# Optimization experiments

Hardware: AMD Instinct MI355X
Metric: run time of the kernel (lower is better)

The kernel has to match this reference:

```python
import jax, jax.numpy as jnp
import numpy as np

NEG_INF = -1000000.0  # matches the original's -1e6 masking constant


def setup_inputs() -> dict:
    key = jax.random.key(0)
    ks = jax.random.split(key, 7)
    B, S, A, Q, D = 32, 2048, 1024, 1024, 1024  # batch, src len, attend_dim, query_dim, att_dim
    return {
        "input": jax.random.normal(ks[0], (B, 1, Q), dtype=jnp.float32),
        "context": jax.random.normal(ks[1], (B, S, A), dtype=jnp.float32),
        "W_pre": jax.random.normal(ks[2], (D, A), dtype=jnp.float32) * 0.02,
        "b_pre": jax.random.normal(ks[3], (D,), dtype=jnp.float32) * 0.02,
        "W_q": jax.random.normal(ks[4], (D, Q), dtype=jnp.float32) * 0.02,
        "v": jax.random.normal(ks[5], (D,), dtype=jnp.float32) * 0.02,
        "mask": jax.random.randint(ks[6], (B, 1, S), 0, 2, dtype=jnp.int32),
    }


def reference(input, context, W_pre, b_pre, W_q, v, mask):
    # precompute = linear_pre(context): [B, S, D]
    precompute = jnp.einsum("bsa,da->bsd", context, W_pre) + b_pre
    # targetT = linear_q(input): [B, 1, D]; repeat over S via broadcast
    targetT = jnp.einsum("bqc,dc->bqd", input, W_q)
    tmp = jnp.tanh(precompute + targetT)                 # [B, S, D]
    energy = jnp.einsum("bsd,d->bs", tmp, v)             # linear_v -> [B, S]
    # mask: positions where mask == 0 get -1e6 (energy*(1-m) + m*(-1e6), m = (mask==0))
    masked_out = (mask[:, 0, :] == 0)
    energy = jnp.where(masked_out, NEG_INF, energy)
    score = jax.nn.softmax(energy, axis=1)               # softmax over S
    score_m = score[:, None, :]                          # [B, 1, S]
    weightedContext = jnp.einsum("bqs,bsa->bqa", score_m, context)  # [B, 1, A]
    return weightedContext, score_m, precompute
```

## Files before the change

### kernel.cpp

```cpp
#include <hip/hip_runtime.h>

#define NEG_INF_VAL -1000000.0f

typedef short s16x8 __attribute__((ext_vector_type(8)));
typedef float f32x4 __attribute__((ext_vector_type(4)));

__device__ __forceinline__ unsigned int bf16_rne(float f) {
  unsigned int u = __float_as_uint(f);
  return (u + 0x7fffu + ((u >> 16) & 1u)) >> 16;
}
__device__ __forceinline__ unsigned int pack_bf2(float a, float b) {
  return bf16_rne(a) | (bf16_rne(b) << 16);
}

__device__ __forceinline__ float fast_tanh(float x) {
  float xc = fminf(fmaxf(x, -15.f), 15.f);
  float t = __expf(2.f * xc);
  return __fdividef(t - 1.f, t + 1.f);
}

__global__ __launch_bounds__(256) void convert_bf16_kernel(
    const float* __restrict__ src, unsigned short* __restrict__ dst, long n) {
  long i = ((long)blockIdx.x * blockDim.x + threadIdx.x) * 8;
  long stride = (long)gridDim.x * blockDim.x * 8;
  for (; i < n; i += stride) {
    float4 f0 = *(const float4*)(src + i);
    float4 f1 = *(const float4*)(src + i + 4);
    uint4 o;
    o.x = pack_bf2(f0.x, f0.y);
    o.y = pack_bf2(f0.z, f0.w);
    o.z = pack_bf2(f1.x, f1.y);
    o.w = pack_bf2(f1.z, f1.w);
    *(uint4*)(dst + i) = o;
  }
}

__global__ __launch_bounds__(256) void targetT_kernel(
    const float* __restrict__ input, const float* __restrict__ Wq,
    float* __restrict__ tT) {
  int d0 = blockIdx.x * 8;
  int t = threadIdx.x;
  int b = t >> 3, dl = t & 7;
  __shared__ float in_s[32][32];
  __shared__ float wq_s[8][32];
  float acc = 0.f;
  for (int q0 = 0; q0 < 1024; q0 += 32) {
    int r = t >> 3, c = (t & 7) * 4;
    *(float4*)&in_s[r][c] = *(const float4*)&input[r * 1024 + q0 + c];
    wq_s[t >> 5][t & 31] = Wq[(long)(d0 + (t >> 5)) * 1024 + q0 + (t & 31)];
    __syncthreads();
#pragma unroll
    for (int qq = 0; qq < 32; ++qq)
      acc += in_s[b][qq] * wq_s[dl][qq];
    __syncthreads();
  }
  tT[b * 1024 + d0 + dl] = acc;
}

__device__ __forceinline__ void load_lds16(const void* g, void* l) {
  __builtin_amdgcn_global_load_lds(
      (const __attribute__((address_space(1))) void*)g,
      (__attribute__((address_space(3))) void*)l, 16, 0, 0);
}

#define MFMA_ROW(QI, I, AF)                                                          \
  acc[(QI)*4+(I)][0] = __builtin_amdgcn_mfma_f32_16x16x32_bf16(AF, bf0, acc[(QI)*4+(I)][0], 0, 0, 0); \
  acc[(QI)*4+(I)][1] = __builtin_amdgcn_mfma_f32_16x16x32_bf16(AF, bf1, acc[(QI)*4+(I)][1], 0, 0, 0); \
  acc[(QI)*4+(I)][2] = __builtin_amdgcn_mfma_f32_16x16x32_bf16(AF, bf2, acc[(QI)*4+(I)][2], 0, 0, 0); \
  acc[(QI)*4+(I)][3] = __builtin_amdgcn_mfma_f32_16x16x32_bf16(AF, bf3, acc[(QI)*4+(I)][3], 0, 0, 0);

#define STAGE(SB, SM, SK, SKTREL)                                                    \
  {                                                                                  \
    const unsigned short* gp = ((SM) ? Bg : Ag) + (SKTREL) * 64 + (SK) * 32;         \
    char* lp = dstB + (SB) * 65536 + (SM) * 32768 + (SK) * 16384;                    \
    load_lds16(gp, lp);                                                              \
    load_lds16(gp + 128L * 1024, lp + 8192);                                         \
  }

#define PHASE(BUF, QI, KK, LOADB, SB, SM, SK, SKTREL, VM)                            \
  {                                                                                  \
    const unsigned short* pA = (BUF) ? pA1 : pA0;                                    \
    const unsigned short* pB = (BUF) ? pB1 : pB0;                                    \
    s16x8 af0 = *(const s16x8*)(pA + (KK)*8192 + ((QI)*64 +  0)*32);                 \
    s16x8 af1 = *(const s16x8*)(pA + (KK)*8192 + ((QI)*64 + 16)*32);                 \
    s16x8 af2 = *(const s16x8*)(pA + (KK)*8192 + ((QI)*64 + 32)*32);                 \
    s16x8 af3 = *(const s16x8*)(pA + (KK)*8192 + ((QI)*64 + 48)*32);                 \
    if (LOADB) {                                                                     \
      bf0 = *(const s16x8*)(pB + (KK)*8192 +  0*32);                                 \
      bf1 = *(const s16x8*)(pB + (KK)*8192 + 16*32);                                 \
      bf2 = *(const s16x8*)(pB + (KK)*8192 + 32*32);                                 \
      bf3 = *(const s16x8*)(pB + (KK)*8192 + 48*32);                                 \
    }                                                                                \
    STAGE(SB, SM, SK, SKTREL)                                                        \
    asm volatile("s_waitcnt lgkmcnt(0)" ::: "memory");                               \
    __builtin_amdgcn_sched_barrier(0);                                               \
    __builtin_amdgcn_s_setprio(1);                                                   \
    MFMA_ROW(QI, 0, af0)                                                             \
    MFMA_ROW(QI, 1, af1)                                                             \
    MFMA_ROW(QI, 2, af2)                                                             \
    MFMA_ROW(QI, 3, af3)                                                             \
    __builtin_amdgcn_s_setprio(0);                                                   \
    if (VM) asm volatile("s_waitcnt vmcnt(8)" ::: "memory");                         \
    __builtin_amdgcn_s_barrier();                                                    \
  }

__global__ __launch_bounds__(512, 2) void gemm_energy_kernel(
    const unsigned short* __restrict__ A,
    const unsigned short* __restrict__ Bm,
    const float* __restrict__ b_pre,
    const float* __restrict__ tT,
    const float* __restrict__ vvec,
    float* __restrict__ Cout,
    float* __restrict__ epart) {
  int lin = blockIdx.x;
  int w = (lin & 7) * 128 + (lin >> 3);
  int nt = w & 3;
  int mt = w >> 2;
  int m0 = mt * 256, n0 = nt * 256;
  int tid = threadIdx.x;
  int lane = tid & 63, wid = tid >> 6;
  int wr = wid >> 2, wc = wid & 3;
  int r = lane & 15, g = lane >> 4;

  __shared__ unsigned short sMem[2 * 2 * 2 * 256 * 32];

  f32x4 acc[8][4] = {};
  s16x8 bf0, bf1, bf2, bf3;

  int physoff = (g ^ ((r >> 1) & 3)) * 8;

  int aoffe = (wr * 128 + r) * 32 + physoff;
  int boffe = (wc * 64 + r) * 32 + physoff;
  const unsigned short* pA0 = sMem + aoffe;
  const unsigned short* pA1 = sMem + 32768 + aoffe;
  const unsigned short* pB0 = sMem + 16384 + boffe;
  const unsigned short* pB1 = sMem + 49152 + boffe;
  char* dstB = (char*)sMem + wid * 1024;

  int srow = tid >> 2;
  int slog8 = ((tid & 3) ^ ((tid >> 3) & 3)) * 8;
  const unsigned short* Abase = A + (long)(m0 + srow) * 1024 + slog8;
  const unsigned short* Bbase = Bm + (long)(n0 + srow) * 1024 + slog8;
  const unsigned short* Ag = Abase;
  const unsigned short* Bg = Bbase;

  STAGE(0, 0, 0, 0) STAGE(0, 1, 0, 0)
  STAGE(0, 0, 1, 0) STAGE(0, 1, 1, 0)
  STAGE(1, 0, 0, 1) STAGE(1, 1, 0, 1)
  asm volatile("s_waitcnt vmcnt(8)" ::: "memory");
  __builtin_amdgcn_s_barrier();

#pragma unroll 1
  for (int t0 = 0; t0 < 16; t0 += 2) {
    Ag = Abase + t0 * 64;
    Bg = Bbase + t0 * 64;
    PHASE(0, 0, 0, 1, 1, 0, 1, 1, 0)
    PHASE(0, 1, 0, 0, 1, 1, 1, 1, 1)
    PHASE(0, 0, 1, 1, 0, 0, 0, 2, 0)
    PHASE(0, 1, 1, 0, 0, 1, 0, 2, 1)
    PHASE(1, 0, 0, 1, 0, 0, 1, 2, 0)
    PHASE(1, 1, 0, 0, 0, 1, 1, 2, 1)
    PHASE(1, 0, 1, 1, 1, 0, 0, 3, 0)
    PHASE(1, 1, 1, 0, 1, 1, 0, 3, 1)
  }

  int b = m0 >> 11;
  float bias[4], tv[4], vv[4];
#pragma unroll
  for (int j = 0; j < 4; ++j) {
    int d = n0 + wc * 64 + j * 16 + r;
    bias[j] = b_pre[d];
    tv[j] = tT[b * 1024 + d];
    vv[j] = vvec[d];
  }
#pragma unroll
  for (int i = 0; i < 8; ++i) {
#pragma unroll
    for (int q = 0; q < 4; ++q) {
      int m = m0 + wr * 128 + i * 16 + g * 4 + q;
      float e = 0.f;
#pragma unroll
      for (int j = 0; j < 4; ++j) {
        float val = acc[i][j][q] + bias[j];
        Cout[(long)m * 1024 + n0 + wc * 64 + j * 16 + r] = val;
        e += fast_tanh(val + tv[j]) * vv[j];
      }
      e += __shfl_xor(e, 1);
      e += __shfl_xor(e, 2);
      e += __shfl_xor(e, 4);
      e += __shfl_xor(e, 8);
      if (r == 0) epart[(long)m * 16 + nt * 4 + wc] = e;
    }
  }
}

__global__ __launch_bounds__(256) void softmax_kernel(
    const float* __restrict__ epart, const int* __restrict__ mask,
    float* __restrict__ score) {
  int b = blockIdx.x;
  int t = threadIdx.x;
  __shared__ float red[256];
  float ev[8];
  float mx = -3.4e38f;
#pragma unroll
  for (int ii = 0; ii < 8; ++ii) {
    int s = ii * 256 + t;
    long m = (long)b * 2048 + s;
    const float4* p = (const float4*)(epart + m * 16);
    float4 p0 = p[0], p1 = p[1], p2 = p[2], p3 = p[3];
    float e = p0.x + p0.y + p0.z + p0.w + p1.x + p1.y + p1.z + p1.w
            + p2.x + p2.y + p2.z + p2.w + p3.x + p3.y + p3.z + p3.w;
    if (mask[b * 2048 + s] == 0) e = NEG_INF_VAL;
    ev[ii] = e;
    mx = fmaxf(mx, e);
  }
  red[t] = mx; __syncthreads();
  for (int off = 128; off > 0; off >>= 1) {
    if (t < off) red[t] = fmaxf(red[t], red[t + off]);
    __syncthreads();
  }
  mx = red[0];
  __syncthreads();
  float sum = 0.f;
#pragma unroll
  for (int ii = 0; ii < 8; ++ii) { ev[ii] = __expf(ev[ii] - mx); sum += ev[ii]; }
  red[t] = sum; __syncthreads();
  for (int off = 128; off > 0; off >>= 1) {
    if (t < off) red[t] += red[t + off];
    __syncthreads();
  }
  float inv = 1.f / red[0];
#pragma unroll
  for (int ii = 0; ii < 8; ++ii)
    score[b * 2048 + ii * 256 + t] = ev[ii] * inv;
}

__global__ __launch_bounds__(256) void wc_partial_kernel(
    const unsigned short* __restrict__ ctx, const float* __restrict__ score,
    float* __restrict__ part) {
  int b = blockIdx.x, sc = blockIdx.y;
  int t = threadIdx.x;
  __shared__ float ssc[64];
  if (t < 64) ssc[t] = score[b * 2048 + sc * 64 + t];
  __syncthreads();
  float acc0 = 0.f, acc1 = 0.f, acc2 = 0.f, acc3 = 0.f;
  const unsigned short* cp = ctx + ((long)b * 2048 + sc * 64) * 1024 + t * 4;
  for (int s = 0; s < 64; ++s) {
    uint2 pk = *(const uint2*)cp;
    cp += 1024;
    float wgt = ssc[s];
    acc0 += wgt * __uint_as_float(pk.x << 16);
    acc1 += wgt * __uint_as_float(pk.x & 0xffff0000u);
    acc2 += wgt * __uint_as_float(pk.y << 16);
    acc3 += wgt * __uint_as_float(pk.y & 0xffff0000u);
  }
  float* pp = part + ((long)(b * 32 + sc)) * 1024 + t * 4;
  pp[0] = acc0; pp[1] = acc1; pp[2] = acc2; pp[3] = acc3;
}

__global__ __launch_bounds__(256) void wc_reduce_kernel(
    const float* __restrict__ part, float* __restrict__ wc) {
  int id = blockIdx.x * 256 + threadIdx.x;
  int b = id >> 10, a = id & 1023;
  float s = 0.f;
#pragma unroll
  for (int scn = 0; scn < 32; ++scn)
    s += part[((long)(b * 32 + scn)) * 1024 + a];
  wc[id] = s;
}

extern "C" void kernel_launch(void* const* d_in, const int* in_sizes, int n_in,
                              void* d_out, int out_size, void* d_ws, size_t ws_size,
                              hipStream_t stream) {
  const float* input   = (const float*)d_in[0];
  const float* context = (const float*)d_in[1];
  const float* W_pre   = (const float*)d_in[2];
  const float* b_pre   = (const float*)d_in[3];
  const float* W_q     = (const float*)d_in[4];
  const float* v       = (const float*)d_in[5];
  const int*   mask    = (const int*)d_in[6];

  float* out       = (float*)d_out;
  float* out_wc    = out;
  float* out_score = out + 32768;
  float* out_pre   = out + 98304;

  const size_t OFF_CTX   = 0;
  const size_t OFF_WPRE  = 134217728;
  const size_t OFF_TT    = 136314880;
  const size_t OFF_EPART = 136445952;
  const size_t OFF_WCP   = 140640256;
  const size_t WS_NEED   = 144834560;
  if (ws_size < WS_NEED) return;

  char* ws = (char*)d_ws;
  unsigned short* ctx_bf  = (unsigned short*)(ws + OFF_CTX);
  unsigned short* wpre_bf = (unsigned short*)(ws + OFF_WPRE);
  float* tT     = (float*)(ws + OFF_TT);
  float* epart  = (float*)(ws + OFF_EPART);
  float* wcpart = (float*)(ws + OFF_WCP);

  convert_bf16_kernel<<<2048, 256, 0, stream>>>(context, ctx_bf, 64LL * 1024 * 1024);
  convert_bf16_kernel<<<256, 256, 0, stream>>>(W_pre, wpre_bf, 1024LL * 1024);
  targetT_kernel<<<128, 256, 0, stream>>>(input, W_q, tT);
  gemm_energy_kernel<<<1024, 512, 0, stream>>>(ctx_bf, wpre_bf, b_pre, tT, v,
                                               out_pre, epart);
  softmax_kernel<<<32, 256, 0, stream>>>(epart, mask, out_score);
  dim3 g5(32, 32);
  wc_partial_kernel<<<g5, 256, 0, stream>>>(ctx_bf, out_score, wcpart);
  wc_reduce_kernel<<<128, 256, 0, stream>>>(wcpart, out_wc);
}
```

Before: 339.8 us.

## Software-pipeline LDS fragment reads one phase ahead of MFMAs in GEMM

Restructures the GEMM main loop so that A/B fragments for the next phase are read from LDS into a second register set while the MFMAs of the current phase run. This removes the explicit lgkmcnt(0) wait and sched_barrier before each MFMA block, hiding LDS latency behind compute. The global-to-LDS prefetch wait is also loosened from vmcnt(8) to vmcnt(4), and a final vmcnt(0) is added after the loop. The cost is more VGPRs for the double fragment sets, which risks spills or reduced occupancy under the 512x2 launch bounds, and correctness depends on the barrier ordering now that reads run one phase ahead.

```diff
diff --git a/kernel.cpp b/kernel.cpp
--- a/kernel.cpp
+++ b/kernel.cpp
@@ -63,44 +63,44 @@
       (__attribute__((address_space(3))) void*)l, 16, 0, 0);
 }
 
-#define MFMA_ROW(QI, I, AF)                                                          \
-  acc[(QI)*4+(I)][0] = __builtin_amdgcn_mfma_f32_16x16x32_bf16(AF, bf0, acc[(QI)*4+(I)][0], 0, 0, 0); \
-  acc[(QI)*4+(I)][1] = __builtin_amdgcn_mfma_f32_16x16x32_bf16(AF, bf1, acc[(QI)*4+(I)][1], 0, 0, 0); \
-  acc[(QI)*4+(I)][2] = __builtin_amdgcn_mfma_f32_16x16x32_bf16(AF, bf2, acc[(QI)*4+(I)][2], 0, 0, 0); \
-  acc[(QI)*4+(I)][3] = __builtin_amdgcn_mfma_f32_16x16x32_bf16(AF, bf3, acc[(QI)*4+(I)][3], 0, 0, 0);
-
-#define STAGE(SB, SM, SK, SKTREL)                                                    \
+#define RD_A(SET, BUF, KK, QI)                                                       \
+  SET##_0 = *(const s16x8*)(((BUF) ? pA1 : pA0) + (KK)*8192 + ((QI)*64 +  0)*32);    \
+  SET##_1 = *(const s16x8*)(((BUF) ? pA1 : pA0) + (KK)*8192 + ((QI)*64 + 16)*32);    \
+  SET##_2 = *(const s16x8*)(((BUF) ? pA1 : pA0) + (KK)*8192 + ((QI)*64 + 32)*32);    \
+  SET##_3 = *(const s16x8*)(((BUF) ? pA1 : pA0) + (KK)*8192 + ((QI)*64 + 48)*32);
+
+#define RD_B(SET, BUF, KK)                                                           \
+  SET##_0 = *(const s16x8*)(((BUF) ? pB1 : pB0) + (KK)*8192 +  0*32);                \
+  SET##_1 = *(const s16x8*)(((BUF) ? pB1 : pB0) + (KK)*8192 + 16*32);                \
+  SET##_2 = *(const s16x8*)(((BUF) ? pB1 : pB0) + (KK)*8192 + 32*32);                \
+  SET##_3 = *(const s16x8*)(((BUF) ? pB1 : pB0) + (KK)*8192 + 48*32);
+
+#define MFMA_ROW(QI, I, AF, BS)                                                      \
+  acc[(QI)*4+(I)][0] = __builtin_amdgcn_mfma_f32_16x16x32_bf16(AF, BS##_0, acc[(QI)*4+(I)][0], 0, 0, 0); \
+  acc[(QI)*4+(I)][1] = __builtin_amdgcn_mfma_f32_16x16x32_bf16(AF, BS##_1, acc[(QI)*4+(I)][1], 0, 0, 0); \
+  acc[(QI)*4+(I)][2] = __builtin_amdgcn_mfma_f32_16x16x32_bf16(AF, BS##_2, acc[(QI)*4+(I)][2], 0, 0, 0); \
+  acc[(QI)*4+(I)][3] = __builtin_amdgcn_mfma_f32_16x16x32_bf16(AF, BS##_3, acc[(QI)*4+(I)][3], 0, 0, 0);
+
+#define STAGE(SB, SM, SK, SKT)                                                       \
   {                                                                                  \
-    const unsigned short* gp = ((SM) ? Bg : Ag) + (SKTREL) * 64 + (SK) * 32;         \
+    const unsigned short* gp = ((SM) ? Bg : Ag) + (SKT) * 64 + (SK) * 32;            \
     char* lp = dstB + (SB) * 65536 + (SM) * 32768 + (SK) * 16384;                    \
     load_lds16(gp, lp);                                                              \
     load_lds16(gp + 128L * 1024, lp + 8192);                                         \
   }
 
-#define PHASE(BUF, QI, KK, LOADB, SB, SM, SK, SKTREL, VM)                            \
+#define PHASE(CQI, CAS, CBS, RAB, RAK, RAQ, RAS, RLB, RBB, RBK, RBS, SB, SM, SK, SKT, VM) \
   {                                                                                  \
-    const unsigned short* pA = (BUF) ? pA1 : pA0;                                    \
-    const unsigned short* pB = (BUF) ? pB1 : pB0;                                    \
-    s16x8 af0 = *(const s16x8*)(pA + (KK)*8192 + ((QI)*64 +  0)*32);                 \
-    s16x8 af1 = *(const s16x8*)(pA + (KK)*8192 + ((QI)*64 + 16)*32);                 \
-    s16x8 af2 = *(const s16x8*)(pA + (KK)*8192 + ((QI)*64 + 32)*32);                 \
-    s16x8 af3 = *(const s16x8*)(pA + (KK)*8192 + ((QI)*64 + 48)*32);                 \
-    if (LOADB) {                                                                     \
-      bf0 = *(const s16x8*)(pB + (KK)*8192 +  0*32);                                 \
-      bf1 = *(const s16x8*)(pB + (KK)*8192 + 16*32);                                 \
-      bf2 = *(const s16x8*)(pB + (KK)*8192 + 32*32);                                 \
-      bf3 = *(const s16x8*)(pB + (KK)*8192 + 48*32);                                 \
-    }                                                                                \
-    STAGE(SB, SM, SK, SKTREL)                                                        \
-    asm volatile("s_waitcnt lgkmcnt(0)" ::: "memory");                               \
-    __builtin_amdgcn_sched_barrier(0);                                               \
+    RD_A(RAS, RAB, RAK, RAQ)                                                         \
+    if (RLB) { RD_B(RBS, RBB, RBK) }                                                 \
+    STAGE(SB, SM, SK, SKT)                                                           \
     __builtin_amdgcn_s_setprio(1);                                                   \
-    MFMA_ROW(QI, 0, af0)                                                             \
-    MFMA_ROW(QI, 1, af1)                                                             \
-    MFMA_ROW(QI, 2, af2)                                                             \
-    MFMA_ROW(QI, 3, af3)                                                             \
+    MFMA_ROW(CQI, 0, CAS##_0, CBS)                                                   \
+    MFMA_ROW(CQI, 1, CAS##_1, CBS)                                                   \
+    MFMA_ROW(CQI, 2, CAS##_2, CBS)                                                   \
+    MFMA_ROW(CQI, 3, CAS##_3, CBS)                                                   \
     __builtin_amdgcn_s_setprio(0);                                                   \
-    if (VM) asm volatile("s_waitcnt vmcnt(8)" ::: "memory");                         \
+    if (VM) asm volatile("s_waitcnt vmcnt(4)" ::: "memory");                         \
     __builtin_amdgcn_s_barrier();                                                    \
   }
 
@@ -125,7 +125,8 @@
   __shared__ unsigned short sMem[2 * 2 * 2 * 256 * 32];
 
   f32x4 acc[8][4] = {};
-  s16x8 bf0, bf1, bf2, bf3;
+  s16x8 a0_0{}, a0_1{}, a0_2{}, a0_3{}, a1_0{}, a1_1{}, a1_2{}, a1_3{};
+  s16x8 b0_0{}, b0_1{}, b0_2{}, b0_3{}, b1_0{}, b1_1{}, b1_2{}, b1_3{};
 
   int physoff = (g ^ ((r >> 1) & 3)) * 8;
 
@@ -147,22 +148,25 @@
   STAGE(0, 0, 0, 0) STAGE(0, 1, 0, 0)
   STAGE(0, 0, 1, 0) STAGE(0, 1, 1, 0)
   STAGE(1, 0, 0, 1) STAGE(1, 1, 0, 1)
-  asm volatile("s_waitcnt vmcnt(8)" ::: "memory");
+  asm volatile("s_waitcnt vmcnt(4)" ::: "memory");
   __builtin_amdgcn_s_barrier();
+  RD_A(a0, 0, 0, 0)
+  RD_B(b0, 0, 0)
 
 #pragma unroll 1
   for (int t0 = 0; t0 < 16; t0 += 2) {
     Ag = Abase + t0 * 64;
     Bg = Bbase + t0 * 64;
-    PHASE(0, 0, 0, 1, 1, 0, 1, 1, 0)
-    PHASE(0, 1, 0, 0, 1, 1, 1, 1, 1)
-    PHASE(0, 0, 1, 1, 0, 0, 0, 2, 0)
-    PHASE(0, 1, 1, 0, 0, 1, 0, 2, 1)
-    PHASE(1, 0, 0, 1, 0, 0, 1, 2, 0)
-    PHASE(1, 1, 0, 0, 0, 1, 1, 2, 1)
-    PHASE(1, 0, 1, 1, 1, 0, 0, 3, 0)
-    PHASE(1, 1, 1, 0, 1, 1, 0, 3, 1)
-  }
+    PHASE(0, a0, b0,  0, 0, 1, a1,   0, 0, 0, b1,   1, 0, 1, 1, 0)
+    PHASE(1, a1, b0,  0, 1, 0, a0,   1, 0, 1, b1,   1, 1, 1, 1, 1)
+    PHASE(0, a0, b1,  0, 1, 1, a1,   0, 0, 0, b0,   0, 0, 0, 2, 0)
+    PHASE(1, a1, b1,  1, 0, 0, a0,   1, 1, 0, b0,   0, 1, 0, 2, 1)
+    PHASE(0, a0, b0,  1, 0, 1, a1,   0, 0, 0, b1,   0, 0, 1, 2, 0)
+    PHASE(1, a1, b0,  1, 1, 0, a0,   1, 1, 1, b1,   0, 1, 1, 2, 1)
+    PHASE(0, a0, b1,  1, 1, 1, a1,   0, 0, 0, b0,   1, 0, 0, 3, 0)
+    PHASE(1, a1, b1,  0, 0, 0, a0,   1, 0, 0, b0,   1, 1, 0, 3, 1)
+  }
+  asm volatile("s_waitcnt vmcnt(0)" ::: "memory");
 
   int b = m0 >> 11;
   float bias[4], tv[4], vv[4];
```

After: 340.3 us. No clear change (+0.1%).
